# Optimization experiments

Hardware: AMD Instinct MI355X
Metric: run time of the kernel (lower is better)

The kernel has to match this reference:

```python
import jax, jax.numpy as jnp
import numpy as np

B, N, C = 16, 1024, 768
H = 12
HD = C // H
MLP = 4 * C
EPS = 1e-5  # torch nn.LayerNorm default
LS_INIT = 1e-5


def _ln(x, g, b):
    mu = jnp.mean(x, axis=-1, keepdims=True)
    var = jnp.var(x, axis=-1, keepdims=True)
    return (x - mu) * jax.lax.rsqrt(var + EPS) * g + b


def setup_inputs() -> dict:
    key = jax.random.key(0)
    ks = jax.random.split(key, 8)
    s = 0.02
    return {
        "x": jax.random.normal(ks[0], (B, N, C), dtype=jnp.float32),
        "w_qkv": jax.random.normal(ks[1], (C, 3 * C), dtype=jnp.float32) * s,
        "w_proj": jax.random.normal(ks[2], (C, C), dtype=jnp.float32) * s,
        "b_proj": jnp.zeros((C,), jnp.float32),
        "ln1_g": jnp.ones((C,), jnp.float32),
        "ln1_b": jnp.zeros((C,), jnp.float32),
        "ln2_g": jnp.ones((C,), jnp.float32),
        "ln2_b": jnp.zeros((C,), jnp.float32),
        "ls1_g": jnp.full((C,), LS_INIT, jnp.float32),
        "ls2_g": jnp.full((C,), LS_INIT, jnp.float32),
        "w_fc1": jax.random.normal(ks[3], (C, MLP), dtype=jnp.float32) * s,
        "b_fc1": jnp.zeros((MLP,), jnp.float32),
        "w_fc2": jax.random.normal(ks[4], (MLP, C), dtype=jnp.float32) * s,
        "b_fc2": jnp.zeros((C,), jnp.float32),
    }


def reference(x, w_qkv, w_proj, b_proj, ln1_g, ln1_b, ln2_g, ln2_b,
              ls1_g, ls2_g, w_fc1, b_fc1, w_fc2, b_fc2):
    scale = HD ** -0.5
    # ---- attention branch (pre-norm) ----
    h = x
    y = _ln(x, ln1_g, ln1_b)
    qkv = (y @ w_qkv).reshape(B, N, 3, H, HD)
    q, k, v = (jnp.moveaxis(qkv, 2, 0)[i].transpose(0, 2, 1, 3) for i in range(3))  # [B,H,N,HD]
    attn = jnp.einsum("bhnd,bhmd->bhnm", q * scale, k)
    attn = attn - jnp.max(attn, axis=-1, keepdims=True)  # explicit max-subtract as in source
    attn = jax.nn.softmax(attn, axis=-1)
    o = jnp.einsum("bhnm,bhmd->bhnd", attn, v).transpose(0, 2, 1, 3).reshape(B, N, C)
    o = o @ w_proj + b_proj
    x = h + o * ls1_g  # LayerScale (fp32)
    # ---- MLP branch ----
    h = x
    y = _ln(x, ln2_g, ln2_b)
    y = jax.nn.gelu(y @ w_fc1 + b_fc1, approximate=False)
    y = y @ w_fc2 + b_fc2
    x = h + y * ls2_g
    return x  # weights=None since vis=False
```

## Files before the change

### kernel.cpp

```cpp
#include <hip/hip_runtime.h>
#include <cstdint>
#include <cstddef>

typedef __bf16 bf16;
typedef __bf16 bf16x4 __attribute__((ext_vector_type(4)));
typedef __bf16 bf16x8 __attribute__((ext_vector_type(8)));
typedef _Float16 f16;
typedef _Float16 f16x4 __attribute__((ext_vector_type(4)));
typedef _Float16 f16x8 __attribute__((ext_vector_type(8)));
typedef float  f32x4  __attribute__((ext_vector_type(4)));
typedef unsigned char u8;

#define B_   16
#define N_   1024
#define C_   768
#define H_   12
#define HD_  64
#define M_   (B_*N_)
#define MLP_ 3072
#define QKVN 2304
#define WSCALE 64.0f
#define WINV  (1.0f/64.0f)

__device__ __forceinline__ void gll16(const void* g, void* l) {
  __builtin_amdgcn_global_load_lds((const __attribute__((address_space(1))) void*)g,
                                   (__attribute__((address_space(3))) void*)l,
                                   16, 0, 0);
}

__device__ __forceinline__ float fast_exp2(float x) { return __builtin_amdgcn_exp2f(x); }
__device__ __forceinline__ float fast_rcp(float x)  { return __builtin_amdgcn_rcpf(x); }

__device__ __forceinline__ u8 to_fp8(float a) {
  return (u8)(__builtin_amdgcn_cvt_pk_fp8_f32(a, a, 0, false) & 0xff);
}
__device__ __forceinline__ int to_fp8x4(float v0, float v1, float v2, float v3) {
  int p = __builtin_amdgcn_cvt_pk_fp8_f32(v0, v1, 0, false);
  p = __builtin_amdgcn_cvt_pk_fp8_f32(v2, v3, p, true);
  return p;
}

__global__ void transpose_cast(const float* __restrict__ w, u8* __restrict__ wt,
                               int K, int N) {
  __shared__ float tile[32][33];
  int n0 = blockIdx.x * 32, k0 = blockIdx.y * 32;
  int tx = threadIdx.x, ty = threadIdx.y;
  #pragma unroll
  for (int i = 0; i < 32; i += 8)
    tile[ty + i][tx] = w[(size_t)(k0 + ty + i) * N + n0 + tx];
  __syncthreads();
  #pragma unroll
  for (int i = 0; i < 32; i += 8)
    wt[(size_t)(n0 + ty + i) * K + k0 + tx] = to_fp8(tile[tx][ty + i] * WSCALE);
}

__global__ __launch_bounds__(256)
void ln_cast_kernel(const float* __restrict__ x, const float* __restrict__ g,
                    const float* __restrict__ bta, u8* __restrict__ y) {
  int row = blockIdx.x;
  int tid = threadIdx.x;
  const float* xr = x + (size_t)row * C_;
  float v0 = xr[tid], v1 = xr[tid + 256], v2 = xr[tid + 512];
  float s  = v0 + v1 + v2;
  float sq = v0 * v0 + v1 * v1 + v2 * v2;
  #pragma unroll
  for (int off = 32; off > 0; off >>= 1) {
    s  += __shfl_xor(s,  off);
    sq += __shfl_xor(sq, off);
  }
  __shared__ float red[8];
  int wave = tid >> 6, lane = tid & 63;
  if (lane == 0) { red[wave] = s; red[4 + wave] = sq; }
  __syncthreads();
  s  = red[0] + red[1] + red[2] + red[3];
  sq = red[4] + red[5] + red[6] + red[7];
  float mean = s * (1.0f / C_);
  float var  = sq * (1.0f / C_) - mean * mean;
  float rstd = rsqrtf(var + 1e-5f);
  u8* yr = y + (size_t)row * C_;
  yr[tid]       = to_fp8((v0 - mean) * rstd * g[tid]       + bta[tid]);
  yr[tid + 256] = to_fp8((v1 - mean) * rstd * g[tid + 256] + bta[tid + 256]);
  yr[tid + 512] = to_fp8((v2 - mean) * rstd * g[tid + 512] + bta[tid + 512]);
}

template <int EPI>
__global__ __launch_bounds__(256)
void gemm_bt(const u8* __restrict__ A, const u8* __restrict__ Bt,
             void* __restrict__ outp, const float* __restrict__ bias,
             const float* __restrict__ ls, const float* __restrict__ resid,
             int M, int N, int K, int nb) {
  constexpr int BM = 128, BN = 128, BK = 64;
  __shared__ __align__(16) u8 As[2][BM * BK];
  __shared__ __align__(16) u8 Bs[2][BM * BK];
  int tid  = threadIdx.x;
  int lane = tid & 63, wave = tid >> 6;
  int quad = lane >> 4, l16 = lane & 15;
  int bid = blockIdx.x;
  int xcd = bid & 7, seq = bid >> 3;
  int mi = xcd + 8 * (seq / nb), ni = seq % nb;
  int m0 = mi * BM, n0 = ni * BN;
  int wm = (wave >> 1) * 64, wn = (wave & 1) * 64;

  const u8* ag[2]; const u8* bg[2];
  #pragma unroll
  for (int s = 0; s < 2; s++) {
    int u = tid + s * 256;
    int r = u >> 2, g = (u & 3) ^ ((r >> 1) & 3);
    ag[s] = A  + (size_t)(m0 + r) * K + g * 16;
    bg[s] = Bt + (size_t)(n0 + r) * K + g * 16;
  }
  int swz = (l16 >> 1) & 3;

  const f32x4 fz = {0.f, 0.f, 0.f, 0.f};
  f32x4 acc[4][4];
  #pragma unroll
  for (int i = 0; i < 4; i++)
    #pragma unroll
    for (int j = 0; j < 4; j++) acc[i][j] = fz;

  gll16(ag[0], &As[0][0] + tid * 16);
  gll16(ag[1], &As[0][0] + 4096 + tid * 16);
  gll16(bg[0], &Bs[0][0] + tid * 16);
  gll16(bg[1], &Bs[0][0] + 4096 + tid * 16);

  int buf = 0;
  for (int k0 = 0; k0 < K; k0 += BK) {
    __syncthreads();
    if (k0 + BK < K) {
      gll16(ag[0] + k0 + BK, &As[buf ^ 1][0] + tid * 16);
      gll16(ag[1] + k0 + BK, &As[buf ^ 1][0] + 4096 + tid * 16);
      gll16(bg[0] + k0 + BK, &Bs[buf ^ 1][0] + tid * 16);
      gll16(bg[1] + k0 + BK, &Bs[buf ^ 1][0] + 4096 + tid * 16);
    }
    #pragma unroll
    for (int kk = 0; kk < 2; kk++) {
      int go = (((kk << 1) | (quad >> 1)) ^ swz) * 16 + (quad & 1) * 8;
      long af[4], bfr[4];
      #pragma unroll
      for (int i = 0; i < 4; i++)
        af[i] = *(const long*)(&As[buf][0] + (wm + i * 16 + l16) * 64 + go);
      #pragma unroll
      for (int j = 0; j < 4; j++)
        bfr[j] = *(const long*)(&Bs[buf][0] + (wn + j * 16 + l16) * 64 + go);
      #pragma unroll
      for (int i = 0; i < 4; i++)
        #pragma unroll
        for (int j = 0; j < 4; j++)
          acc[i][j] = __builtin_amdgcn_mfma_f32_16x16x32_fp8_fp8(af[i], bfr[j],
                                                                 acc[i][j], 0, 0, 0);
    }
    buf ^= 1;
  }

  #pragma unroll
  for (int i = 0; i < 4; i++) {
    int rowb = m0 + wm + i * 16 + quad * 4;
    #pragma unroll
    for (int j = 0; j < 4; j++) {
      int col = n0 + wn + j * 16 + l16;
      float bias_c = (EPI == 0) ? 0.f : bias[col];
      float ls_c   = (EPI == 1 || EPI == 3) ? ls[col] : 0.f;
      float gz_v = -2.45546696f * WINV;
      float gz_b = -2.45546696f * bias_c;
      #pragma unroll
      for (int r = 0; r < 4; r++) {
        float v = acc[i][j][r];
        size_t idx = (size_t)(rowb + r) * N + col;
        if constexpr (EPI == 0) {
          ((bf16*)outp)[idx] = (bf16)(v * WINV);
        } else if constexpr (EPI == 1) {
          float t = fmaf(v, WINV, bias_c);
          ((float*)outp)[idx] = fmaf(t, ls_c, resid[idx]);
        } else if constexpr (EPI == 2) {
          float t  = fmaf(v, WINV, bias_c);
          float zn = fmaf(v, gz_v, gz_b);
          float gv = t * fast_rcp(1.0f + fast_exp2(zn));
          ((u8*)outp)[idx] = to_fp8(gv);
        } else {
          float t = fmaf(v, WINV, bias_c);
          ((float*)outp)[idx] = fmaf(t, ls_c, resid[idx]);
        }
      }
    }
  }
}

__global__ void transpose_v(const bf16* __restrict__ qkv, f16* __restrict__ vt) {
  __shared__ bf16 tile[32][33];
  int bh = blockIdx.z;
  int b = bh / H_, h = bh % H_;
  int n0 = blockIdx.x * 32, d0 = blockIdx.y * 32;
  int tx = threadIdx.x, ty = threadIdx.y;
  const bf16* src = qkv + (size_t)(b * N_) * QKVN + 2 * C_ + h * HD_;
  #pragma unroll
  for (int i = 0; i < 32; i += 8)
    tile[ty + i][tx] = src[(size_t)(n0 + ty + i) * QKVN + d0 + tx];
  __syncthreads();
  f16* dst = vt + (size_t)bh * HD_ * N_;
  #pragma unroll
  for (int i = 0; i < 32; i += 8)
    dst[(size_t)(d0 + ty + i) * N_ + n0 + tx] = (f16)(float)tile[tx][ty + i];
}

__global__ __launch_bounds__(256)
void attn_kernel(const bf16* __restrict__ qkv, const f16* __restrict__ vt,
                 u8* __restrict__ o) {
  constexpr int KSTR = 72;
  constexpr int VSTR = 136;
  __shared__ __align__(16) bf16 Ks[128 * KSTR];
  __shared__ __align__(16) f16  Vs[HD_ * VSTR];

  int tid = threadIdx.x, lane = tid & 63, wave = tid >> 6;
  int quad = lane >> 4, l16 = lane & 15;
  int bid = blockIdx.x;
  int xcd = bid & 7, seq = bid >> 3;
  int bh = xcd + 8 * (seq >> 3);
  int b = bh / H_, h = bh % H_;
  int q0 = (seq & 7) * 128;
  const float CEXP = 0.125f * 1.44269504f;

  bf16x8 qf[2][2];
  #pragma unroll
  for (int i = 0; i < 2; i++)
    #pragma unroll
    for (int kk = 0; kk < 2; kk++)
      qf[i][kk] = *(const bf16x8*)(qkv + (size_t)(b * N_ + q0 + wave * 32 + i * 16 + l16) * QKVN
                                   + h * HD_ + kk * 32 + quad * 8);

  const f32x4 fz = {0.f, 0.f, 0.f, 0.f};
  f32x4 oacc[2][4];
  float m_run[2], l_run[2];
  #pragma unroll
  for (int i = 0; i < 2; i++) {
    #pragma unroll
    for (int jd = 0; jd < 4; jd++) oacc[i][jd] = fz;
    m_run[i] = -1e30f; l_run[i] = 0.f;
  }

  const bf16* kbase = qkv + (size_t)(b * N_) * QKVN + C_ + h * HD_;
  const f16*  vbase = vt + (size_t)bh * HD_ * N_;

  int kr[4], kc[4], vr[4], vc[4];
  #pragma unroll
  for (int u = 0; u < 4; u++) {
    int L = tid + u * 256;
    kr[u] = L >> 3;  kc[u] = (L & 7) * 8;
    vr[u] = L >> 4;  vc[u] = (L & 15) * 8;
  }

  bf16x8 kreg[4]; f16x8 vreg[4];
  #pragma unroll
  for (int u = 0; u < 4; u++) {
    kreg[u] = *(const bf16x8*)(kbase + (size_t)kr[u] * QKVN + kc[u]);
    vreg[u] = *(const f16x8*)(vbase + (size_t)vr[u] * N_ + vc[u]);
  }

  for (int kv = 0; kv < N_; kv += 128) {
    __syncthreads();
    #pragma unroll
    for (int u = 0; u < 4; u++) {
      *(bf16x8*)(Ks + kr[u] * KSTR + kc[u]) = kreg[u];
      *(f16x8*)(Vs + vr[u] * VSTR + vc[u])  = vreg[u];
    }
    __syncthreads();

    if (kv + 128 < N_) {
      #pragma unroll
      for (int u = 0; u < 4; u++) {
        kreg[u] = *(const bf16x8*)(kbase + (size_t)(kv + 128 + kr[u]) * QKVN + kc[u]);
        vreg[u] = *(const f16x8*)(vbase + (size_t)vr[u] * N_ + kv + 128 + vc[u]);
      }
    }

    f32x4 sv[2][8];
    #pragma unroll
    for (int i = 0; i < 2; i++)
      #pragma unroll
      for (int kf = 0; kf < 8; kf++) sv[i][kf] = fz;
    #pragma unroll
    for (int kk = 0; kk < 2; kk++) {
      #pragma unroll
      for (int kf = 0; kf < 8; kf++) {
        bf16x8 kb = *(const bf16x8*)(Ks + (kf * 16 + l16) * KSTR + kk * 32 + quad * 8);
        sv[0][kf] = __builtin_amdgcn_mfma_f32_16x16x32_bf16(kb, qf[0][kk], sv[0][kf], 0, 0, 0);
        sv[1][kf] = __builtin_amdgcn_mfma_f32_16x16x32_bf16(kb, qf[1][kk], sv[1][kf], 0, 0, 0);
      }
    }

    f16x4 pb[2][8];
    #pragma unroll
    for (int i = 0; i < 2; i++) {
      float mx = sv[i][0][0];
      #pragma unroll
      for (int kf = 0; kf < 8; kf++)
        #pragma unroll
        for (int r = 0; r < 4; r++) mx = fmaxf(mx, sv[i][kf][r]);
      mx = fmaxf(mx, __shfl_xor(mx, 16));
      mx = fmaxf(mx, __shfl_xor(mx, 32));
      float mold = m_run[i];
      float mnew = fmaxf(mold, mx);
      float mb   = mnew * CEXP;
      float al   = fast_exp2(mold * CEXP - mb);
      float rs = 0.f;
      #pragma unroll
      for (int kf = 0; kf < 8; kf++) {
        #pragma unroll
        for (int r = 0; r < 4; r++) {
          float p = fast_exp2(sv[i][kf][r] * CEXP - mb);
          pb[i][kf][r] = (f16)p;
          rs += p;
        }
      }
      rs += __shfl_xor(rs, 16);
      rs += __shfl_xor(rs, 32);
      m_run[i] = mnew;
      l_run[i] = l_run[i] * al + rs;
      #pragma unroll
      for (int jd = 0; jd < 4; jd++) oacc[i][jd] *= al;
    }

    #pragma unroll
    for (int kc2 = 0; kc2 < 8; kc2++) {
      #pragma unroll
      for (int jd = 0; jd < 4; jd++) {
        f16x4 va = *(const f16x4*)(Vs + (jd * 16 + l16) * VSTR + kc2 * 16 + quad * 4);
        oacc[0][jd] = __builtin_amdgcn_mfma_f32_16x16x16f16(va, pb[0][kc2], oacc[0][jd], 0, 0, 0);
        oacc[1][jd] = __builtin_amdgcn_mfma_f32_16x16x16f16(va, pb[1][kc2], oacc[1][jd], 0, 0, 0);
      }
    }
  }

  #pragma unroll
  for (int i = 0; i < 2; i++) {
    float inv = fast_rcp(l_run[i]);
    int n = q0 + wave * 32 + i * 16 + l16;
    #pragma unroll
    for (int jd = 0; jd < 4; jd++) {
      int p = to_fp8x4(oacc[i][jd][0] * inv, oacc[i][jd][1] * inv,
                       oacc[i][jd][2] * inv, oacc[i][jd][3] * inv);
      *(int*)(o + (size_t)(b * N_ + n) * C_ + h * HD_ + jd * 16 + quad * 4) = p;
    }
  }
}

#define WQKVT_OFF  0u
#define WPROJT_OFF 1769472u
#define WFC1T_OFF  2359296u
#define WFC2T_OFF  4718592u
#define Y_OFF      7077888u
#define QKV_OFF    19660800u
#define VT_OFF     95158272u
#define O_OFF      120324096u
#define X1_OFF     132907008u
#define WS_NEEDED  183238656u

extern "C" void kernel_launch(void* const* d_in, const int* in_sizes, int n_in,
                              void* d_out, int out_size, void* d_ws, size_t ws_size,
                              hipStream_t stream) {
  if (ws_size < (size_t)WS_NEEDED) return;

  const float* x      = (const float*)d_in[0];
  const float* w_qkv  = (const float*)d_in[1];
  const float* w_proj = (const float*)d_in[2];
  const float* b_proj = (const float*)d_in[3];
  const float* ln1_g  = (const float*)d_in[4];
  const float* ln1_b  = (const float*)d_in[5];
  const float* ln2_g  = (const float*)d_in[6];
  const float* ln2_b  = (const float*)d_in[7];
  const float* ls1_g  = (const float*)d_in[8];
  const float* ls2_g  = (const float*)d_in[9];
  const float* w_fc1  = (const float*)d_in[10];
  const float* b_fc1  = (const float*)d_in[11];
  const float* w_fc2  = (const float*)d_in[12];
  const float* b_fc2  = (const float*)d_in[13];

  char* ws = (char*)d_ws;
  u8*    wqkvT  = (u8*)(ws + WQKVT_OFF);
  u8*    wprojT = (u8*)(ws + WPROJT_OFF);
  u8*    wfc1T  = (u8*)(ws + WFC1T_OFF);
  u8*    wfc2T  = (u8*)(ws + WFC2T_OFF);
  u8*    y      = (u8*)(ws + Y_OFF);
  bf16*  qkv    = (bf16*)(ws + QKV_OFF);
  u8*    hbuf   = (u8*)(ws + QKV_OFF);
  f16*   vt     = (f16*)(ws + VT_OFF);
  u8*    o      = (u8*)(ws + O_OFF);
  float* x1     = (float*)(ws + X1_OFF);
  float* out    = (float*)d_out;

  dim3 tb(32, 8);
  transpose_cast<<<dim3(QKVN / 32, C_ / 32), tb, 0, stream>>>(w_qkv,  wqkvT,  C_,   QKVN);
  transpose_cast<<<dim3(C_   / 32, C_ / 32), tb, 0, stream>>>(w_proj, wprojT, C_,   C_);
  transpose_cast<<<dim3(MLP_ / 32, C_ / 32), tb, 0, stream>>>(w_fc1,  wfc1T,  C_,   MLP_);
  transpose_cast<<<dim3(C_ / 32, MLP_ / 32), tb, 0, stream>>>(w_fc2,  wfc2T,  MLP_, C_);

  ln_cast_kernel<<<M_, 256, 0, stream>>>(x, ln1_g, ln1_b, y);

  gemm_bt<0><<<(QKVN / 128) * 128, 256, 0, stream>>>(
      y, wqkvT, qkv, nullptr, nullptr, nullptr, M_, QKVN, C_, QKVN / 128);

  transpose_v<<<dim3(N_ / 32, HD_ / 32, B_ * H_), tb, 0, stream>>>(qkv, vt);

  attn_kernel<<<(N_ / 128) * B_ * H_, 256, 0, stream>>>(qkv, vt, o);

  gemm_bt<1><<<(C_ / 128) * 128, 256, 0, stream>>>(
      o, wprojT, x1, b_proj, ls1_g, x, M_, C_, C_, C_ / 128);

  ln_cast_kernel<<<M_, 256, 0, stream>>>(x1, ln2_g, ln2_b, y);

  gemm_bt<2><<<(MLP_ / 128) * 128, 256, 0, stream>>>(
      y, wfc1T, hbuf, b_fc1, nullptr, nullptr, M_, MLP_, C_, MLP_ / 128);

  gemm_bt<3><<<(C_ / 128) * 128, 256, 0, stream>>>(
      hbuf, wfc2T, out, b_fc2, ls2_g, x1, M_, C_, MLP_, C_ / 128);
}
```

Baseline: 500.4 us.

## Fuse weight prep with LN1, skew GEMM K-loop and attention KV start

Merges the four weight transpose-cast launches and the first LayerNorm cast into one prep kernel, removing four launches and letting the small jobs share the GPU. The GEMM K-loop now starts at a different K offset for each column block, and attention blocks start their KV sweep at different tiles by query tile. The skews spread concurrent blocks across different addresses to reduce channel or cache contention. The rotated summation order changes floating-point rounding slightly.

```diff
diff --git a/kernel.cpp b/kernel.cpp
--- a/kernel.cpp
+++ b/kernel.cpp
@@ -40,11 +40,18 @@
   return p;
 }
 
-__global__ void transpose_cast(const float* __restrict__ w, u8* __restrict__ wt,
-                               int K, int N) {
+#define T_QKV  1728
+#define T_PROJ 2304
+#define T_FC1  4608
+#define T_FC2  6912
+#define T_ALL  6912
+
+__device__ __forceinline__ void tc_tile(const float* __restrict__ w, u8* __restrict__ wt,
+                                        int K, int N, int t, int tid) {
   __shared__ float tile[32][33];
-  int n0 = blockIdx.x * 32, k0 = blockIdx.y * 32;
-  int tx = threadIdx.x, ty = threadIdx.y;
+  int tiles_n = N >> 5;
+  int n0 = (t % tiles_n) * 32, k0 = (t / tiles_n) * 32;
+  int tx = tid & 31, ty = tid >> 5;
   #pragma unroll
   for (int i = 0; i < 32; i += 8)
     tile[ty + i][tx] = w[(size_t)(k0 + ty + i) * N + n0 + tx];
@@ -52,6 +59,47 @@
   #pragma unroll
   for (int i = 0; i < 32; i += 8)
     wt[(size_t)(n0 + ty + i) * K + k0 + tx] = to_fp8(tile[tx][ty + i] * WSCALE);
+}
+
+__global__ __launch_bounds__(256)
+void prep_kernel(const float* __restrict__ x,
+                 const float* __restrict__ w_qkv, const float* __restrict__ w_proj,
+                 const float* __restrict__ w_fc1, const float* __restrict__ w_fc2,
+                 const float* __restrict__ g, const float* __restrict__ bta,
+                 u8* __restrict__ wqkvT, u8* __restrict__ wprojT,
+                 u8* __restrict__ wfc1T, u8* __restrict__ wfc2T,
+                 u8* __restrict__ y) {
+  int bid = blockIdx.x, tid = threadIdx.x;
+  if (bid < T_ALL) {
+    if (bid < T_QKV)       tc_tile(w_qkv,  wqkvT,  C_,   QKVN, bid,          tid);
+    else if (bid < T_PROJ) tc_tile(w_proj, wprojT, C_,   C_,   bid - T_QKV,  tid);
+    else if (bid < T_FC1)  tc_tile(w_fc1,  wfc1T,  C_,   MLP_, bid - T_PROJ, tid);
+    else                   tc_tile(w_fc2,  wfc2T,  MLP_, C_,   bid - T_FC1,  tid);
+    return;
+  }
+  int row = bid - T_ALL;
+  const float* xr = x + (size_t)row * C_;
+  float v0 = xr[tid], v1 = xr[tid + 256], v2 = xr[tid + 512];
+  float s  = v0 + v1 + v2;
+  float sq = v0 * v0 + v1 * v1 + v2 * v2;
+  #pragma unroll
+  for (int off = 32; off > 0; off >>= 1) {
+    s  += __shfl_xor(s,  off);
+    sq += __shfl_xor(sq, off);
+  }
+  __shared__ float red[8];
+  int wave = tid >> 6, lane = tid & 63;
+  if (lane == 0) { red[wave] = s; red[4 + wave] = sq; }
+  __syncthreads();
+  s  = red[0] + red[1] + red[2] + red[3];
+  sq = red[4] + red[5] + red[6] + red[7];
+  float mean = s * (1.0f / C_);
+  float var  = sq * (1.0f / C_) - mean * mean;
+  float rstd = rsqrtf(var + 1e-5f);
+  u8* yr = y + (size_t)row * C_;
+  yr[tid]       = to_fp8((v0 - mean) * rstd * g[tid]       + bta[tid]);
+  yr[tid + 256] = to_fp8((v1 - mean) * rstd * g[tid + 256] + bta[tid + 256]);
+  yr[tid + 512] = to_fp8((v2 - mean) * rstd * g[tid + 512] + bta[tid + 512]);
 }
 
 __global__ __launch_bounds__(256)
@@ -101,6 +149,9 @@
   int m0 = mi * BM, n0 = ni * BN;
   int wm = (wave >> 1) * 64, wn = (wave & 1) * 64;
 
+  int iters = K >> 6;
+  int skew  = (ni * iters) / nb;
+
   const u8* ag[2]; const u8* bg[2];
   #pragma unroll
   for (int s = 0; s < 2; s++) {
@@ -118,19 +169,25 @@
     #pragma unroll
     for (int j = 0; j < 4; j++) acc[i][j] = fz;
 
-  gll16(ag[0], &As[0][0] + tid * 16);
-  gll16(ag[1], &As[0][0] + 4096 + tid * 16);
-  gll16(bg[0], &Bs[0][0] + tid * 16);
-  gll16(bg[1], &Bs[0][0] + 4096 + tid * 16);
+  int kidx = skew;
+  {
+    int k0 = kidx * BK;
+    gll16(ag[0] + k0, &As[0][0] + tid * 16);
+    gll16(ag[1] + k0, &As[0][0] + 4096 + tid * 16);
+    gll16(bg[0] + k0, &Bs[0][0] + tid * 16);
+    gll16(bg[1] + k0, &Bs[0][0] + 4096 + tid * 16);
+  }
 
   int buf = 0;
-  for (int k0 = 0; k0 < K; k0 += BK) {
+  for (int it = 0; it < iters; it++) {
     __syncthreads();
-    if (k0 + BK < K) {
-      gll16(ag[0] + k0 + BK, &As[buf ^ 1][0] + tid * 16);
-      gll16(ag[1] + k0 + BK, &As[buf ^ 1][0] + 4096 + tid * 16);
-      gll16(bg[0] + k0 + BK, &Bs[buf ^ 1][0] + tid * 16);
-      gll16(bg[1] + k0 + BK, &Bs[buf ^ 1][0] + 4096 + tid * 16);
+    int knext = kidx + 1; if (knext == iters) knext = 0;
+    if (it + 1 < iters) {
+      int kn = knext * BK;
+      gll16(ag[0] + kn, &As[buf ^ 1][0] + tid * 16);
+      gll16(ag[1] + kn, &As[buf ^ 1][0] + 4096 + tid * 16);
+      gll16(bg[0] + kn, &Bs[buf ^ 1][0] + tid * 16);
+      gll16(bg[1] + kn, &Bs[buf ^ 1][0] + 4096 + tid * 16);
     }
     #pragma unroll
     for (int kk = 0; kk < 2; kk++) {
@@ -149,6 +206,7 @@
           acc[i][j] = __builtin_amdgcn_mfma_f32_16x16x32_fp8_fp8(af[i], bfr[j],
                                                                  acc[i][j], 0, 0, 0);
     }
+    kidx = knext;
     buf ^= 1;
   }
 
@@ -216,7 +274,8 @@
   int xcd = bid & 7, seq = bid >> 3;
   int bh = xcd + 8 * (seq >> 3);
   int b = bh / H_, h = bh % H_;
-  int q0 = (seq & 7) * 128;
+  int qt = seq & 7;
+  int q0 = qt * 128;
   const float CEXP = 0.125f * 1.44269504f;
 
   bf16x8 qf[2][2];
@@ -249,13 +308,16 @@
   }
 
   bf16x8 kreg[4]; f16x8 vreg[4];
-  #pragma unroll
-  for (int u = 0; u < 4; u++) {
-    kreg[u] = *(const bf16x8*)(kbase + (size_t)kr[u] * QKVN + kc[u]);
-    vreg[u] = *(const f16x8*)(vbase + (size_t)vr[u] * N_ + vc[u]);
-  }
-
-  for (int kv = 0; kv < N_; kv += 128) {
+  {
+    int kv = qt * 128;
+    #pragma unroll
+    for (int u = 0; u < 4; u++) {
+      kreg[u] = *(const bf16x8*)(kbase + (size_t)(kv + kr[u]) * QKVN + kc[u]);
+      vreg[u] = *(const f16x8*)(vbase + (size_t)vr[u] * N_ + kv + vc[u]);
+    }
+  }
+
+  for (int t = 0; t < 8; t++) {
     __syncthreads();
     #pragma unroll
     for (int u = 0; u < 4; u++) {
@@ -264,11 +326,12 @@
     }
     __syncthreads();
 
-    if (kv + 128 < N_) {
+    if (t + 1 < 8) {
+      int kv = ((t + 1 + qt) & 7) * 128;
       #pragma unroll
       for (int u = 0; u < 4; u++) {
-        kreg[u] = *(const bf16x8*)(kbase + (size_t)(kv + 128 + kr[u]) * QKVN + kc[u]);
-        vreg[u] = *(const f16x8*)(vbase + (size_t)vr[u] * N_ + kv + 128 + vc[u]);
+        kreg[u] = *(const bf16x8*)(kbase + (size_t)(kv + kr[u]) * QKVN + kc[u]);
+        vreg[u] = *(const f16x8*)(vbase + (size_t)vr[u] * N_ + kv + vc[u]);
       }
     }
 
@@ -387,17 +450,14 @@
   float* x1     = (float*)(ws + X1_OFF);
   float* out    = (float*)d_out;
 
-  dim3 tb(32, 8);
-  transpose_cast<<<dim3(QKVN / 32, C_ / 32), tb, 0, stream>>>(w_qkv,  wqkvT,  C_,   QKVN);
-  transpose_cast<<<dim3(C_   / 32, C_ / 32), tb, 0, stream>>>(w_proj, wprojT, C_,   C_);
-  transpose_cast<<<dim3(MLP_ / 32, C_ / 32), tb, 0, stream>>>(w_fc1,  wfc1T,  C_,   MLP_);
-  transpose_cast<<<dim3(C_ / 32, MLP_ / 32), tb, 0, stream>>>(w_fc2,  wfc2T,  MLP_, C_);
-
-  ln_cast_kernel<<<M_, 256, 0, stream>>>(x, ln1_g, ln1_b, y);
+  prep_kernel<<<T_ALL + M_, 256, 0, stream>>>(
+      x, w_qkv, w_proj, w_fc1, w_fc2, ln1_g, ln1_b,
+      wqkvT, wprojT, wfc1T, wfc2T, y);
 
   gemm_bt<0><<<(QKVN / 128) * 128, 256, 0, stream>>>(
       y, wqkvT, qkv, nullptr, nullptr, nullptr, M_, QKVN, C_, QKVN / 128);
 
+  dim3 tb(32, 8);
   transpose_v<<<dim3(N_ / 32, HD_ / 32, B_ * H_), tb, 0, stream>>>(qkv, vt);
 
   attn_kernel<<<(N_ / 128) * B_ * H_, 256, 0, stream>>>(qkv, vt, o);
```

New measurement: 499.6 us. About the same (-0.2%).
